# Kernel tuning notes

Hardware: AMD Instinct MI355X
Metric: run time of the kernel (lower is better)

## Reference

```python
import jax, jax.numpy as jnp
import numpy as np

B, H, S, D = 2, 16, 1024, 64  # batch, n_heads, seq_len, d_k
NEG = -1.0e9


def setup_inputs() -> dict:
    key = jax.random.key(0)
    kq, kk, kv, kt, kf, km, kd = jax.random.split(key, 7)
    Q = jax.random.normal(kq, (B, H, S, D), dtype=jnp.float32)
    K = jax.random.normal(kk, (B, H, S, D), dtype=jnp.float32)
    V = jax.random.normal(kv, (B, H, S, D), dtype=jnp.float32)
    ia_type = jax.random.normal(kt, (B, H, S, S), dtype=jnp.float32)
    ia_feat = jax.random.normal(kf, (B, H, S, S), dtype=jnp.float32)
    attn_mask_if = jax.random.bernoulli(km, 0.1, (B, H, S, S))
    attn_mask = attn_mask_if  # passed to forward but unused, as in the source
    distance_matrix = jax.random.normal(kd, (B, S, S), dtype=jnp.float32)
    return {"Q": Q, "K": K, "V": V, "attn_mask": attn_mask,
            "attn_mask_if": attn_mask_if, "ia_type": ia_type,
            "ia_feat": ia_feat, "distance_matrix": distance_matrix}


def reference(Q, K, V, attn_mask, attn_mask_if, ia_type, ia_feat, distance_matrix):
    # scores1 = Q K^T / sqrt(d_k)
    scores1 = jnp.einsum("bhqd,bhkd->bhqk", Q, K) / jnp.sqrt(jnp.float32(D))
    # bias masked to -1e9, then scores masked again to -1e9 => masked entries are exactly -1e9
    scores = jnp.where(attn_mask_if, NEG, scores1 + ia_type + ia_feat)
    attn = jax.nn.softmax(scores, axis=-1)
    context = jnp.einsum("bhqk,bhkd->bhqd", attn, V)
    return context, attn
```

## Files before the change

### kernel.cpp

```cpp
#include <hip/hip_runtime.h>
#include <math.h>

#define S_LEN 1024
#define D_DIM 64
#define NEGV  (-1.0e9f)

__global__ __launch_bounds__(256, 2)
void attn_bias_fused(const float* __restrict__ Q, const float* __restrict__ K,
                     const float* __restrict__ V, const int* __restrict__ mif,
                     const float* __restrict__ iat, const float* __restrict__ iaf,
                     float* __restrict__ ctx, float* __restrict__ attn)
{
    __shared__ float4 Kt4[D_DIM][64];
    __shared__ float  SB[2048];

    float* Pn = (float*)Kt4;
    float (*Qst)[16] = (float(*)[16])SB;

    const int tid  = threadIdx.x;
    const int wave = tid >> 6;
    const int lane = tid & 63;
    const int bh   = blockIdx.x >> 6;
    const int qb   = (blockIdx.x & 63) << 4;

    const float* Qb = Q + ((size_t)(bh * S_LEN + qb)) * D_DIM;
    const float* Kb = K + ((size_t)bh * S_LEN) * D_DIM;
    const float* Vb = V + ((size_t)bh * S_LEN) * D_DIM;

    {
        int q = tid >> 4, l = tid & 15;
        float4 v = *(const float4*)(Qb + (size_t)q * D_DIM + l * 4);
        Qst[4 * l + 0][q] = v.x;
        Qst[4 * l + 1][q] = v.y;
        Qst[4 * l + 2][q] = v.z;
        Qst[4 * l + 3][q] = v.w;
    }

    const int kg = lane;
    const int qg = wave;

    float4 sc[16];

    #pragma unroll
    for (int c = 0; c < 4; ++c) {
        __syncthreads();
        {
            int l = tid & 15, kr0 = tid >> 4;
            #pragma unroll
            for (int i = 0; i < 16; ++i) {
                int kk = i * 16 + kr0;
                float4 v = *(const float4*)(Kb + (size_t)(c * 256 + kk) * D_DIM + l * 4);
                int cc  = (kk >> 2) ^ (l & 7);
                int sub = kk & 3;
                ((float*)&Kt4[4 * l + 0][cc])[sub] = v.x;
                ((float*)&Kt4[4 * l + 1][cc])[sub] = v.y;
                ((float*)&Kt4[4 * l + 2][cc])[sub] = v.z;
                ((float*)&Kt4[4 * l + 3][cc])[sub] = v.w;
            }
        }
        __syncthreads();

        float4 bt[4], bf[4];
        int4   bm[4];
        #pragma unroll
        for (int i = 0; i < 4; ++i) {
            size_t off = ((size_t)(bh * S_LEN + qb + qg * 4 + i)) * S_LEN + c * 256 + kg * 4;
            bt[i] = *(const float4*)(iat + off);
            bf[i] = *(const float4*)(iaf + off);
            bm[i] = *(const int4*)(mif + off);
        }

        float4 a0 = {0.f, 0.f, 0.f, 0.f}, a1 = a0, a2 = a0, a3 = a0;
        #pragma unroll 16
        for (int d = 0; d < D_DIM; ++d) {
            float4 kv = Kt4[d][kg ^ ((d >> 2) & 7)];
            float4 qv = *(const float4*)&Qst[d][qg * 4];
            a0.x = fmaf(qv.x, kv.x, a0.x); a0.y = fmaf(qv.x, kv.y, a0.y);
            a0.z = fmaf(qv.x, kv.z, a0.z); a0.w = fmaf(qv.x, kv.w, a0.w);
            a1.x = fmaf(qv.y, kv.x, a1.x); a1.y = fmaf(qv.y, kv.y, a1.y);
            a1.z = fmaf(qv.y, kv.z, a1.z); a1.w = fmaf(qv.y, kv.w, a1.w);
            a2.x = fmaf(qv.z, kv.x, a2.x); a2.y = fmaf(qv.z, kv.y, a2.y);
            a2.z = fmaf(qv.z, kv.z, a2.z); a2.w = fmaf(qv.z, kv.w, a2.w);
            a3.x = fmaf(qv.w, kv.x, a3.x); a3.y = fmaf(qv.w, kv.y, a3.y);
            a3.z = fmaf(qv.w, kv.z, a3.z); a3.w = fmaf(qv.w, kv.w, a3.w);
        }

        float4 av[4] = {a0, a1, a2, a3};
        #pragma unroll
        for (int i = 0; i < 4; ++i) {
            float4 s = av[i];
            float4 t = bt[i], f = bf[i];
            int4   m = bm[i];
            s.x = m.x ? NEGV : fmaf(s.x, 0.125f, t.x + f.x);
            s.y = m.y ? NEGV : fmaf(s.y, 0.125f, t.y + f.y);
            s.z = m.z ? NEGV : fmaf(s.z, 0.125f, t.z + f.z);
            s.w = m.w ? NEGV : fmaf(s.w, 0.125f, t.w + f.w);
            sc[c * 4 + i] = s;
        }
    }
    __syncthreads();

    {
        float mx[4], sum[4], rinv[4];
        #pragma unroll
        for (int i = 0; i < 4; ++i) {
            float m = -INFINITY;
            #pragma unroll
            for (int c = 0; c < 4; ++c) {
                float4 v = sc[c * 4 + i];
                m = fmaxf(m, fmaxf(fmaxf(v.x, v.y), fmaxf(v.z, v.w)));
            }
            #pragma unroll
            for (int s = 1; s < 64; s <<= 1) m = fmaxf(m, __shfl_xor(m, s, 64));
            mx[i] = m;
        }
        #pragma unroll
        for (int i = 0; i < 4; ++i) {
            float sm = 0.f;
            #pragma unroll
            for (int c = 0; c < 4; ++c) {
                float4 v = sc[c * 4 + i];
                v.x = __expf(v.x - mx[i]);
                v.y = __expf(v.y - mx[i]);
                v.z = __expf(v.z - mx[i]);
                v.w = __expf(v.w - mx[i]);
                sc[c * 4 + i] = v;
                sm += v.x + v.y + v.z + v.w;
            }
            #pragma unroll
            for (int s = 1; s < 64; s <<= 1) sm += __shfl_xor(sm, s, 64);
            sum[i] = sm;
            rinv[i] = 1.f / sm;
        }
        #pragma unroll
        for (int i = 0; i < 4; ++i) {
            int r = qg * 4 + i;
            float* arow = attn + ((size_t)(bh * S_LEN + qb + r)) * S_LEN;
            #pragma unroll
            for (int c = 0; c < 4; ++c) {
                float4 v = sc[c * 4 + i];
                v.x *= rinv[i]; v.y *= rinv[i]; v.z *= rinv[i]; v.w *= rinv[i];
                *(float4*)(arow + c * 256 + kg * 4)  = v;
                *(float4*)&Pn[r * 1024 + c * 256 + kg * 4] = v;
            }
        }
        (void)sum;
    }
    __syncthreads();

    {
        int dg = lane & 15;
        int ks = lane >> 4;
        float4 acc[16];
        #pragma unroll
        for (int q = 0; q < 16; ++q) acc[q] = make_float4(0.f, 0.f, 0.f, 0.f);

        #pragma unroll 2
        for (int i = 0; i < 16; ++i) {
            int k0 = wave * 256 + i * 16 + ks * 4;
            const float* vrow = Vb + (size_t)k0 * D_DIM + dg * 4;
            float4 v0 = *(const float4*)(vrow + 0 * D_DIM);
            float4 v1 = *(const float4*)(vrow + 1 * D_DIM);
            float4 v2 = *(const float4*)(vrow + 2 * D_DIM);
            float4 v3 = *(const float4*)(vrow + 3 * D_DIM);
            #pragma unroll
            for (int q = 0; q < 16; ++q) {
                float4 p = *(const float4*)&Pn[q * 1024 + k0];
                float4 a = acc[q];
                a.x = fmaf(p.x, v0.x, a.x); a.x = fmaf(p.y, v1.x, a.x);
                a.x = fmaf(p.z, v2.x, a.x); a.x = fmaf(p.w, v3.x, a.x);
                a.y = fmaf(p.x, v0.y, a.y); a.y = fmaf(p.y, v1.y, a.y);
                a.y = fmaf(p.z, v2.y, a.y); a.y = fmaf(p.w, v3.y, a.y);
                a.z = fmaf(p.x, v0.z, a.z); a.z = fmaf(p.y, v1.z, a.z);
                a.z = fmaf(p.z, v2.z, a.z); a.z = fmaf(p.w, v3.z, a.z);
                a.w = fmaf(p.x, v0.w, a.w); a.w = fmaf(p.y, v1.w, a.w);
                a.w = fmaf(p.z, v2.w, a.w); a.w = fmaf(p.w, v3.w, a.w);
                acc[q] = a;
            }
        }

        #pragma unroll
        for (int q = 0; q < 16; ++q) {
            acc[q].x += __shfl_xor(acc[q].x, 16, 64);
            acc[q].y += __shfl_xor(acc[q].y, 16, 64);
            acc[q].z += __shfl_xor(acc[q].z, 16, 64);
            acc[q].w += __shfl_xor(acc[q].w, 16, 64);
            acc[q].x += __shfl_xor(acc[q].x, 32, 64);
            acc[q].y += __shfl_xor(acc[q].y, 32, 64);
            acc[q].z += __shfl_xor(acc[q].z, 32, 64);
            acc[q].w += __shfl_xor(acc[q].w, 32, 64);
        }

        float* scratch = SB;
        #pragma unroll
        for (int qh = 0; qh < 2; ++qh) {
            __syncthreads();
            if (lane < 16) {
                #pragma unroll
                for (int j = 0; j < 8; ++j)
                    *(float4*)&scratch[(wave * 8 + j) * 64 + dg * 4] = acc[qh * 8 + j];
            }
            __syncthreads();
            if (tid < 128) {
                int qq = tid >> 4;
                int dr = tid & 15;
                float4 r = make_float4(0.f, 0.f, 0.f, 0.f);
                #pragma unroll
                for (int s = 0; s < 4; ++s) {
                    float4 v = *(const float4*)&scratch[(s * 8 + qq) * 64 + dr * 4];
                    r.x += v.x; r.y += v.y; r.z += v.z; r.w += v.w;
                }
                *(float4*)(ctx + ((size_t)(bh * S_LEN + qb + qh * 8 + qq)) * D_DIM + dr * 4) = r;
            }
        }
    }
}

extern "C" void kernel_launch(void* const* d_in, const int* in_sizes, int n_in,
                              void* d_out, int out_size, void* d_ws, size_t ws_size,
                              hipStream_t stream) {
    const float* Q   = (const float*)d_in[0];
    const float* K   = (const float*)d_in[1];
    const float* V   = (const float*)d_in[2];
    const int*   mif = (const int*)d_in[4];
    const float* iat = (const float*)d_in[5];
    const float* iaf = (const float*)d_in[6];

    float* ctx  = (float*)d_out;
    float* attn = (float*)d_out + (size_t)2 * 16 * 1024 * 64;

    dim3 grid(2048), block(256);
    hipLaunchKernelGGL(attn_bias_fused, grid, block, 0, stream,
                       Q, K, V, mif, iat, iaf, ctx, attn);
}
```

Measured before the change: 538.9 us.

## Store K and probabilities as bf16 in LDS to raise occupancy

The transposed K tile and the normalized probability tile are now kept in shared memory as 16-bit bfloat values: K is truncated and P is rounded to nearest even. They are unpacked back to fp32 for the FMAs. This halves the shared-memory footprint per block, and the launch bounds go from 2 to 4 blocks per CU so more waves can hide global-memory latency on the large bias and mask streams. It lowers the precision of both matmuls, and the tighter register budget may cause spills given the large sc and acc register arrays.

```diff
diff --git a/kernel.cpp b/kernel.cpp
--- a/kernel.cpp
+++ b/kernel.cpp
@@ -5,16 +5,23 @@
 #define D_DIM 64
 #define NEGV  (-1.0e9f)
 
-__global__ __launch_bounds__(256, 2)
+static __device__ inline unsigned short f2bf_rne(float f) {
+    unsigned u = __float_as_uint(f);
+    u += 0x7fffu + ((u >> 16) & 1u);
+    return (unsigned short)(u >> 16);
+}
+
+__global__ __launch_bounds__(256, 4)
 void attn_bias_fused(const float* __restrict__ Q, const float* __restrict__ K,
                      const float* __restrict__ V, const int* __restrict__ mif,
                      const float* __restrict__ iat, const float* __restrict__ iaf,
                      float* __restrict__ ctx, float* __restrict__ attn)
 {
-    __shared__ float4 Kt4[D_DIM][64];
-    __shared__ float  SB[2048];
-
-    float* Pn = (float*)Kt4;
+    __shared__ __align__(16) unsigned short KP[16384];
+    __shared__ float SB[2048];
+
+    unsigned short* Kt = KP;
+    unsigned short* Pn = KP;
     float (*Qst)[16] = (float(*)[16])SB;
 
     const int tid  = threadIdx.x;
@@ -50,12 +57,11 @@
             for (int i = 0; i < 16; ++i) {
                 int kk = i * 16 + kr0;
                 float4 v = *(const float4*)(Kb + (size_t)(c * 256 + kk) * D_DIM + l * 4);
-                int cc  = (kk >> 2) ^ (l & 7);
-                int sub = kk & 3;
-                ((float*)&Kt4[4 * l + 0][cc])[sub] = v.x;
-                ((float*)&Kt4[4 * l + 1][cc])[sub] = v.y;
-                ((float*)&Kt4[4 * l + 2][cc])[sub] = v.z;
-                ((float*)&Kt4[4 * l + 3][cc])[sub] = v.w;
+                int kx = kk ^ (l << 2);
+                Kt[(4 * l + 0) * 256 + kx] = (unsigned short)(__float_as_uint(v.x) >> 16);
+                Kt[(4 * l + 1) * 256 + kx] = (unsigned short)(__float_as_uint(v.y) >> 16);
+                Kt[(4 * l + 2) * 256 + kx] = (unsigned short)(__float_as_uint(v.z) >> 16);
+                Kt[(4 * l + 3) * 256 + kx] = (unsigned short)(__float_as_uint(v.w) >> 16);
             }
         }
         __syncthreads();
@@ -73,16 +79,20 @@
         float4 a0 = {0.f, 0.f, 0.f, 0.f}, a1 = a0, a2 = a0, a3 = a0;
         #pragma unroll 16
         for (int d = 0; d < D_DIM; ++d) {
-            float4 kv = Kt4[d][kg ^ ((d >> 2) & 7)];
+            uint2 u = *(const uint2*)(Kt + d * 256 + (((kg ^ (d >> 2)) << 2)));
+            float k0 = __uint_as_float(u.x << 16);
+            float k1 = __uint_as_float(u.x & 0xffff0000u);
+            float k2 = __uint_as_float(u.y << 16);
+            float k3 = __uint_as_float(u.y & 0xffff0000u);
             float4 qv = *(const float4*)&Qst[d][qg * 4];
-            a0.x = fmaf(qv.x, kv.x, a0.x); a0.y = fmaf(qv.x, kv.y, a0.y);
-            a0.z = fmaf(qv.x, kv.z, a0.z); a0.w = fmaf(qv.x, kv.w, a0.w);
-            a1.x = fmaf(qv.y, kv.x, a1.x); a1.y = fmaf(qv.y, kv.y, a1.y);
-            a1.z = fmaf(qv.y, kv.z, a1.z); a1.w = fmaf(qv.y, kv.w, a1.w);
-            a2.x = fmaf(qv.z, kv.x, a2.x); a2.y = fmaf(qv.z, kv.y, a2.y);
-            a2.z = fmaf(qv.z, kv.z, a2.z); a2.w = fmaf(qv.z, kv.w, a2.w);
-            a3.x = fmaf(qv.w, kv.x, a3.x); a3.y = fmaf(qv.w, kv.y, a3.y);
-            a3.z = fmaf(qv.w, kv.z, a3.z); a3.w = fmaf(qv.w, kv.w, a3.w);
+            a0.x = fmaf(qv.x, k0, a0.x); a0.y = fmaf(qv.x, k1, a0.y);
+            a0.z = fmaf(qv.x, k2, a0.z); a0.w = fmaf(qv.x, k3, a0.w);
+            a1.x = fmaf(qv.y, k0, a1.x); a1.y = fmaf(qv.y, k1, a1.y);
+            a1.z = fmaf(qv.y, k2, a1.z); a1.w = fmaf(qv.y, k3, a1.w);
+            a2.x = fmaf(qv.z, k0, a2.x); a2.y = fmaf(qv.z, k1, a2.y);
+            a2.z = fmaf(qv.z, k2, a2.z); a2.w = fmaf(qv.z, k3, a2.w);
+            a3.x = fmaf(qv.w, k0, a3.x); a3.y = fmaf(qv.w, k1, a3.y);
+            a3.z = fmaf(qv.w, k2, a3.z); a3.w = fmaf(qv.w, k3, a3.w);
         }
 
         float4 av[4] = {a0, a1, a2, a3};
@@ -101,7 +111,7 @@
     __syncthreads();
 
     {
-        float mx[4], sum[4], rinv[4];
+        float mx[4], rinv[4];
         #pragma unroll
         for (int i = 0; i < 4; ++i) {
             float m = -INFINITY;
@@ -129,7 +139,6 @@
             }
             #pragma unroll
             for (int s = 1; s < 64; s <<= 1) sm += __shfl_xor(sm, s, 64);
-            sum[i] = sm;
             rinv[i] = 1.f / sm;
         }
         #pragma unroll
@@ -140,11 +149,13 @@
             for (int c = 0; c < 4; ++c) {
                 float4 v = sc[c * 4 + i];
                 v.x *= rinv[i]; v.y *= rinv[i]; v.z *= rinv[i]; v.w *= rinv[i];
-                *(float4*)(arow + c * 256 + kg * 4)  = v;
-                *(float4*)&Pn[r * 1024 + c * 256 + kg * 4] = v;
-            }
-        }
-        (void)sum;
+                *(float4*)(arow + c * 256 + kg * 4) = v;
+                ushort4 h;
+                h.x = f2bf_rne(v.x); h.y = f2bf_rne(v.y);
+                h.z = f2bf_rne(v.z); h.w = f2bf_rne(v.w);
+                *(ushort4*)&Pn[r * 1024 + c * 256 + kg * 4] = h;
+            }
+        }
     }
     __syncthreads();
 
@@ -165,16 +176,20 @@
             float4 v3 = *(const float4*)(vrow + 3 * D_DIM);
             #pragma unroll
             for (int q = 0; q < 16; ++q) {
-                float4 p = *(const float4*)&Pn[q * 1024 + k0];
+                uint2 up = *(const uint2*)(Pn + q * 1024 + k0);
+                float p0 = __uint_as_float(up.x << 16);
+                float p1 = __uint_as_float(up.x & 0xffff0000u);
+                float p2 = __uint_as_float(up.y << 16);
+                float p3 = __uint_as_float(up.y & 0xffff0000u);
                 float4 a = acc[q];
-                a.x = fmaf(p.x, v0.x, a.x); a.x = fmaf(p.y, v1.x, a.x);
-                a.x = fmaf(p.z, v2.x, a.x); a.x = fmaf(p.w, v3.x, a.x);
-                a.y = fmaf(p.x, v0.y, a.y); a.y = fmaf(p.y, v1.y, a.y);
-                a.y = fmaf(p.z, v2.y, a.y); a.y = fmaf(p.w, v3.y, a.y);
-                a.z = fmaf(p.x, v0.z, a.z); a.z = fmaf(p.y, v1.z, a.z);
-                a.z = fmaf(p.z, v2.z, a.z); a.z = fmaf(p.w, v3.z, a.z);
-                a.w = fmaf(p.x, v0.w, a.w); a.w = fmaf(p.y, v1.w, a.w);
-                a.w = fmaf(p.z, v2.w, a.w); a.w = fmaf(p.w, v3.w, a.w);
+                a.x = fmaf(p0, v0.x, a.x); a.x = fmaf(p1, v1.x, a.x);
+                a.x = fmaf(p2, v2.x, a.x); a.x = fmaf(p3, v3.x, a.x);
+                a.y = fmaf(p0, v0.y, a.y); a.y = fmaf(p1, v1.y, a.y);
+                a.z = fmaf(p0, v0.z, a.z); a.z = fmaf(p1, v1.z, a.z);
+                a.y = fmaf(p2, v2.y, a.y); a.y = fmaf(p3, v3.y, a.y);
+                a.z = fmaf(p2, v2.z, a.z); a.z = fmaf(p3, v3.z, a.z);
+                a.w = fmaf(p0, v0.w, a.w); a.w = fmaf(p1, v1.w, a.w);
+                a.w = fmaf(p2, v2.w, a.w); a.w = fmaf(p3, v3.w, a.w);
                 acc[q] = a;
             }
         }
```

New measurement: 1.265 ms. +134.7%, slower.
